# Kernel optimization log

Measured on AMD Instinct MI355X. Metric: run time of the kernel, lower is better.

Reference implementation:

```python
import jax, jax.numpy as jnp
import numpy as np

N = 256
D = 128
H = 512
EPS_NORM = 1e-12
EPS_COS = 1e-8


def _mlp2(x, w1, b1, w2, b2):
    return jax.nn.relu(x @ w1 + b1) @ w2 + b2


def _l2norm(x):
    n = jnp.sqrt(jnp.sum(x * x, axis=1, keepdims=True))
    return x / jnp.maximum(n, EPS_NORM)


def setup_inputs() -> dict:
    key = jax.random.key(0)
    ks = jax.random.split(key, 20)
    def w(k, shape, fan_in):
        return jax.random.normal(k, shape, dtype=jnp.float32) * (1.0 / np.sqrt(fan_in))
    inp = {
        "graph_1_node": jax.random.normal(ks[0], (N, D), dtype=jnp.float32),
        "graph_2_node": jax.random.normal(ks[1], (N, D), dtype=jnp.float32),
        # Node_embedding: D -> 512 -> D
        "ne_w1": w(ks[2], (D, H), D), "ne_b1": jnp.zeros((H,), jnp.float32),
        "ne_w2": w(ks[3], (H, D), H), "ne_b2": jnp.zeros((D,), jnp.float32),
        # edge_embedding: 2D+2N -> 512 -> D
        "ee_w1": w(ks[4], (2 * D + 2 * N, H), 2 * D + 2 * N), "ee_b1": jnp.zeros((H,), jnp.float32),
        "ee_w2": w(ks[5], (H, D), H), "ee_b2": jnp.zeros((D,), jnp.float32),
        # propagation: 3D -> 512 -> D
        "pr_w1": w(ks[6], (3 * D, H), 3 * D), "pr_b1": jnp.zeros((H,), jnp.float32),
        "pr_w2": w(ks[7], (H, D), H), "pr_b2": jnp.zeros((D,), jnp.float32),
        # update: 3D -> D (single linear)
        "up_w": w(ks[8], (3 * D, D), 3 * D), "up_b": jnp.zeros((D,), jnp.float32),
        # aggregation: 2D -> 1 (single linear, softmax over nodes)
        "ag_w": w(ks[9], (2 * D, 1), 2 * D), "ag_b": jnp.zeros((1,), jnp.float32),
    }
    return inp


def _edge_embed(x, ee_w1, ee_b1, ee_w2, ee_b2):
    # create_edg: per (i,j) concat(x[i], onehot(i), x[j], onehot(j))
    fi = jnp.concatenate([x, jnp.eye(N, dtype=x.dtype)], axis=1)  # [N, D+N]
    ef = jnp.concatenate([
        jnp.broadcast_to(fi[:, None, :], (N, N, D + N)),
        jnp.broadcast_to(fi[None, :, :], (N, N, D + N)),
    ], axis=-1).reshape(N * N, 2 * (D + N))
    return _mlp2(ef, ee_w1, ee_b1, ee_w2, ee_b2).reshape(N, N, D)


def _propagate(x, E, pr_w1, pr_b1, pr_w2, pr_b2):
    # msg[m] = mean_n MLP(cat(x[m], x[n], E[m,n]))
    cat = jnp.concatenate([
        jnp.broadcast_to(x[:, None, :], (N, N, D)),
        jnp.broadcast_to(x[None, :, :], (N, N, D)),
        E,
    ], axis=-1).reshape(N * N, 3 * D)
    msg = _mlp2(cat, pr_w1, pr_b1, pr_w2, pr_b2).reshape(N, N, D)
    return jnp.mean(msg, axis=1)


def _interact(a, b):
    # matching[i] = mean_j b[j] * exp(a[i]*b[j]) / sum_j (a[i]*b[j])
    p = a[:, None, :] * b[None, :, :]                      # [N, N, D]
    w = jnp.exp(p) / jnp.sum(p, axis=1, keepdims=True)
    return jnp.mean(b[None, :, :] * w, axis=1)


def _aggregate(upd, ag_w, ag_b):
    feats = jnp.concatenate([upd, jnp.broadcast_to(jnp.mean(upd, axis=0, keepdims=True), upd.shape)], axis=1)
    s = jax.nn.softmax(feats @ ag_w + ag_b, axis=0)        # [N, 1]
    return jnp.sum(s * upd, axis=0, keepdims=True)          # [1, D]


def reference(graph_1_node, graph_2_node,
              ne_w1, ne_b1, ne_w2, ne_b2,
              ee_w1, ee_b1, ee_w2, ee_b2,
              pr_w1, pr_b1, pr_w2, pr_b2,
              up_w, up_b, ag_w, ag_b):
    emb1 = _mlp2(graph_1_node, ne_w1, ne_b1, ne_w2, ne_b2)
    emb2 = _mlp2(graph_2_node, ne_w1, ne_b1, ne_w2, ne_b2)

    E1 = _edge_embed(graph_1_node, ee_w1, ee_b1, ee_w2, ee_b2)
    E2 = _edge_embed(graph_2_node, ee_w1, ee_b1, ee_w2, ee_b2)

    intra1 = _propagate(graph_1_node, E1, pr_w1, pr_b1, pr_w2, pr_b2)
    intra2 = _propagate(graph_2_node, E2, pr_w1, pr_b1, pr_w2, pr_b2)

    cross1 = _interact(emb1, emb2)
    cross2 = _interact(emb2, emb1)

    upd1 = jnp.concatenate([_l2norm(emb1), _l2norm(intra1), _l2norm(cross1)], axis=1) @ up_w + up_b
    upd2 = jnp.concatenate([_l2norm(emb2), _l2norm(intra2), _l2norm(cross2)], axis=1) @ up_w + up_b

    r1 = _aggregate(upd1, ag_w, ag_b)  # [1, D]
    r2 = _aggregate(upd2, ag_w, ag_b)  # [1, D]

    num = jnp.sum(r1 * r2, axis=1)
    den = jnp.maximum(jnp.linalg.norm(r1, axis=1) * jnp.linalg.norm(r2, axis=1), EPS_COS)
    return (num / den + 1.0) / 2.0
```

## Files before the change

kernel.cpp:

```cpp
#include <hip/hip_runtime.h>
#include <math.h>

#define NN 256
#define DD 128
#define HH 512

#define WS_XW    0
#define WS_XEXT  524288
#define WS_EMB   524288
#define WS_INTRA 589824
#define WS_W4F   720896
#define WS_UPD   720896
#define WS_H1    1114112
#define WS_S     1376256
#define WS_WB5   1638400
#define WS_B4    1802240
#define WS_LGV   1804288

typedef __attribute__((ext_vector_type(8))) _Float16 half8;
typedef __attribute__((ext_vector_type(4))) _Float16 half4v;
typedef __attribute__((ext_vector_type(4))) float f32x4;

__device__ __forceinline__ void gload_lds16(const _Float16* g, _Float16* l) {
  __builtin_amdgcn_global_load_lds(
      (const __attribute__((address_space(1))) unsigned*)g,
      (__attribute__((address_space(3))) unsigned*)l, 16, 0, 0);
}

#define WAITV(N) asm volatile("s_waitcnt vmcnt(" #N ")" ::: "memory")
#define RBARRIER() do { __builtin_amdgcn_s_barrier(); \
                        asm volatile("" ::: "memory"); } while (0)

__global__ void prepk(const float* __restrict__ g1, const float* __restrict__ g2,
                      const float* __restrict__ eew1, const float* __restrict__ prw1,
                      const float* __restrict__ eeb1, const float* __restrict__ prb1,
                      const float* __restrict__ eeb2, const float* __restrict__ eew2,
                      const float* __restrict__ new1, const float* __restrict__ new2,
                      const float* __restrict__ prw2,
                      float* __restrict__ Xext, _Float16* __restrict__ W4f,
                      _Float16* __restrict__ Wb5, float* __restrict__ bias4)
{
  const int b = blockIdx.x, l = threadIdx.x;
  const int low = l & 15, q = l >> 4;
  if (b < 1536) {
    const int f = b;
    const int kcI = f >> 7, ntI = f & 127;
    const int n = ntI * 16 + low, slice = n >> 9, np = n & 511;
    const int kb = kcI * 32 + q * 8;
    half8 v;
    #pragma unroll
    for (int t = 0; t < 8; ++t) {
      const int k = kb + t;
      float val;
      if (slice == 0)      val = eew1[k * HH + np];
      else if (slice == 1) val = eew1[(384 + k) * HH + np];
      else if (slice == 2) val = (k < 128) ? prw1[k * HH + np] : 0.f;
      else                 val = (k < 128) ? prw1[(128 + k) * HH + np] : 0.f;
      v[t] = (_Float16)val;
    }
    *(half8*)&W4f[((size_t)f * 64 + l) * 8] = v;
  } else if (b < 2176) {
    const int idx = b - 1536;
    const int which = idx >> 7, f = idx & 127;
    const float* src; int ld, nt;
    switch (which) {
      case 0:  src = eew2;            ld = 128; nt = 8;  break;
      case 1:  src = prw1 + 256 * HH; ld = 512; nt = 32; break;
      case 2:  src = new1;            ld = 512; nt = 32; break;
      case 3:  src = new2;            ld = 128; nt = 8;  break;
      default: src = prw2;            ld = 128; nt = 8;  break;
    }
    _Float16* dst = Wb5 + (size_t)which * 65536;
    const int kcI = f / nt, ntI = f % nt;
    const int n = ntI * 16 + low;
    const int kb = kcI * 32 + q * 8;
    half8 v;
    #pragma unroll
    for (int t = 0; t < 8; ++t) v[t] = (_Float16)src[(kb + t) * ld + n];
    *(half8*)&dst[((size_t)f * 64 + l) * 8] = v;
  } else if (b < 2688) {
    const int m = b - 2176;
    const int g = m >> 8, i = m & 255;
    const float* src = (g ? g2 : g1) + i * DD;
    float* dst = Xext + (size_t)m * 384;
    #pragma unroll
    for (int c = l; c < 384; c += 64)
      dst[c] = (c < 128) ? src[c] : ((c - 128 == i) ? 1.f : 0.f);
  } else {
    const int n = (b - 2688) * 64 + l;
    float v = 0.f;
    if (n < 512) v = eeb1[n];
    else if (n >= 1024 && n < 1536) {
      const int h = n - 1024;
      float s = prb1[h];
      #pragma unroll 8
      for (int d = 0; d < 128; ++d) s = fmaf(eeb2[d], prw1[(256 + d) * HH + h], s);
      v = s;
    }
    bias4[n] = v;
  }
}

template<int FT, int MT>
__global__ __launch_bounds__(256, 2)
void gemm2(const float* B0, const float* B1, int ldb0, int ldb1,
           float sc0, float sc1,
           const _Float16* A0, const _Float16* A1, int nt0, int nt1,
           int kcn0, int kcn1, const float* bias0, const float* bias1,
           void* O0, void* O1, int ldo0, int ldo1,
           int half0, int half1, int relu0, int relu1, int ylim1)
{
  const int z = blockIdx.z;
  if (z == 1 && (int)blockIdx.y >= ylim1) return;
  const float* Bsrc = z ? B1 : B0;
  const _Float16* Af = z ? A1 : A0;
  const float* bias = z ? bias1 : bias0;
  void* Out = z ? O1 : O0;
  const int ldb = z ? ldb1 : ldb0, ntTot = z ? nt1 : nt0;
  const int kcN = z ? kcn1 : kcn0, ldo = z ? ldo1 : ldo0;
  const int ohalf = z ? half1 : half0, orelu = z ? relu1 : relu0;
  const float sc = z ? sc1 : sc0;

  const int tid = threadIdx.x;
  const int w = tid >> 6, l = tid & 63, low = l & 15, q = l >> 4;
  const int mb = blockIdx.x * (MT * 16);
  const int nb = (blockIdx.y * 4 + w) * (FT * 16);
  f32x4 acc[FT][MT];
  #pragma unroll
  for (int ft = 0; ft < FT; ++ft)
    #pragma unroll
    for (int et = 0; et < MT; ++et) acc[ft][et] = (f32x4){0.f, 0.f, 0.f, 0.f};

  for (int kc = 0; kc < kcN; ++kc) {
    const int k0 = kc * 32 + q * 8;
    half8 bfr[MT];
    #pragma unroll
    for (int et = 0; et < MT; ++et) {
      const float* p = Bsrc + (size_t)(mb + et * 16 + low) * ldb + k0;
      const float4 b0 = *(const float4*)p;
      const float4 b1 = *(const float4*)(p + 4);
      half8 v;
      v[0] = (_Float16)(b0.x * sc); v[1] = (_Float16)(b0.y * sc);
      v[2] = (_Float16)(b0.z * sc); v[3] = (_Float16)(b0.w * sc);
      v[4] = (_Float16)(b1.x * sc); v[5] = (_Float16)(b1.y * sc);
      v[6] = (_Float16)(b1.z * sc); v[7] = (_Float16)(b1.w * sc);
      bfr[et] = v;
    }
    #pragma unroll
    for (int ft = 0; ft < FT; ++ft) {
      const int ng = (nb >> 4) + ft;
      const half8 af = *(const half8*)&Af[((size_t)(kc * ntTot + ng) * 64 + l) * 8];
      #pragma unroll
      for (int et = 0; et < MT; ++et)
        acc[ft][et] = __builtin_amdgcn_mfma_f32_16x16x32_f16(af, bfr[et], acc[ft][et], 0, 0, 0);
    }
  }
  #pragma unroll
  for (int ft = 0; ft < FT; ++ft) {
    const int n0 = nb + ft * 16 + q * 4;
    const float4 bs = *(const float4*)&bias[n0];
    #pragma unroll
    for (int et = 0; et < MT; ++et) {
      const int m = mb + et * 16 + low;
      float vx = acc[ft][et][0] + bs.x;
      float vy = acc[ft][et][1] + bs.y;
      float vz = acc[ft][et][2] + bs.z;
      float vw = acc[ft][et][3] + bs.w;
      if (orelu) {
        vx = fmaxf(vx, 0.f); vy = fmaxf(vy, 0.f);
        vz = fmaxf(vz, 0.f); vw = fmaxf(vw, 0.f);
      }
      if (ohalf) {
        half4v pk;
        pk[0] = (_Float16)vx; pk[1] = (_Float16)vy;
        pk[2] = (_Float16)vz; pk[3] = (_Float16)vw;
        *(half4v*)((_Float16*)Out + (size_t)m * ldo + n0) = pk;
      } else {
        *(float4*)((float*)Out + (size_t)m * ldo + n0) = make_float4(vx, vy, vz, vw);
      }
    }
  }
}

__global__ __launch_bounds__(512, 4)
void heavy_mfma(const _Float16* __restrict__ XW, const _Float16* __restrict__ W2fg,
                const _Float16* __restrict__ WEf, float* __restrict__ SG)
{
  __shared__ _Float16 Ut[128 * DD];
  __shared__ _Float16 Sb[3][4096];
  __shared__ _Float16 AeH[HH];
  __shared__ float PpL[HH];
  __shared__ float Sp[8][HH];
  const int g = blockIdx.z, i = blockIdx.x;
  const int tid = threadIdx.x;
  const _Float16* Xg = XW + (size_t)g * NN * 2048;
  const _Float16* rowI = Xg + (size_t)i * 2048;
  const int w = tid >> 6, l = tid & 63, low = l & 15, q = l >> 4;
  const int xsw = (low & 7) << 1;
  const half8 hz = (half8)((_Float16)0);

  AeH[tid] = rowI[tid];
  PpL[tid] = (float)rowI[1024 + tid];
  #pragma unroll
  for (int t = 0; t < 8; ++t) ((float*)Sp)[tid + t * 512] = 0.f;

  for (int h2 = 0; h2 < 2; ++h2) {
    const int jb = h2 * 128;
    const int j = jb + w * 16 + low;
    const int e = w * 16 + low;

    __syncthreads();
    gload_lds16(W2fg + (size_t)w * 512 + l * 8, &Sb[0][w * 512]);
    gload_lds16(W2fg + 4096 + (size_t)w * 512 + l * 8, &Sb[1][w * 512]);
    {
      half8 ce_cur = *(const half8*)&Xg[(size_t)j * 2048 + 512 + q * 8];
      f32x4 acc[8];
      #pragma unroll
      for (int ct = 0; ct < 8; ++ct) acc[ct] = (f32x4){0.f, 0.f, 0.f, 0.f};
      for (int kc = 0; kc < 16; ++kc) {
        half8 ce_nxt = hz;
        if (kc < 15)
          ce_nxt = *(const half8*)&Xg[(size_t)j * 2048 + 512 + (kc + 1) * 32 + q * 8];
        if (kc == 0)       WAITV(1);
        else if (kc == 15) WAITV(0);
        else               WAITV(2);
        RBARRIER();
        if (kc < 14)
          gload_lds16(W2fg + (size_t)(kc + 2) * 4096 + w * 512 + l * 8,
                      &Sb[(kc + 2) % 3][w * 512]);
        const half8 a = *(const half8*)&AeH[kc * 32 + q * 8];
        const half8 bfr = __builtin_elementwise_max(a + ce_cur, hz);
        const _Float16* sb = &Sb[kc % 3][0];
        __builtin_amdgcn_s_setprio(1);
        #pragma unroll
        for (int ct = 0; ct < 8; ++ct) {
          const half8 wf = *(const half8*)&sb[ct * 512 + l * 8];
          acc[ct] = __builtin_amdgcn_mfma_f32_16x16x32_f16(wf, bfr, acc[ct], 0, 0, 0);
        }
        __builtin_amdgcn_s_setprio(0);
        ce_cur = ce_nxt;
      }
      #pragma unroll
      for (int ct = 0; ct < 8; ++ct) {
        const int cb2 = ct * 4 + q;
        half4v pk;
        pk[0] = (_Float16)acc[ct][0]; pk[1] = (_Float16)acc[ct][1];
        pk[2] = (_Float16)acc[ct][2]; pk[3] = (_Float16)acc[ct][3];
        *(half4v*)&Ut[e * DD + ((cb2 ^ xsw) << 2)] = pk;
      }
    }

    __syncthreads();
    gload_lds16(WEf + (size_t)((w >> 1) * 32 + 0 + (w & 1)) * 512 + l * 8,
                &Sb[0][w * 512]);
    gload_lds16(WEf + (size_t)((w >> 1) * 32 + 2 + (w & 1)) * 512 + l * 8,
                &Sb[1][w * 512]);
    {
      half8 bfr2[4];
      #pragma unroll
      for (int kc2 = 0; kc2 < 4; ++kc2) {
        const int cb0 = kc2 * 8 + q * 2;
        bfr2[kc2] = *(const half8*)&Ut[e * DD + ((cb0 ^ xsw) << 2)];
      }
      const half4v onesv = {(_Float16)1.f, (_Float16)1.f, (_Float16)1.f, (_Float16)1.f};
      for (int cc = 0; cc < 16; ++cc) {
        if (cc == 15) WAITV(0);
        else          WAITV(1);
        RBARRIER();
        const _Float16* sb = &Sb[cc % 3][0];
        #pragma unroll
        for (int t = 0; t < 2; ++t) {
          const int hc = cc * 2 + t;
          const int h0 = hc * 16;
          f32x4 acc2 = (f32x4){0.f, 0.f, 0.f, 0.f};
          __builtin_amdgcn_s_setprio(1);
          #pragma unroll
          for (int kc2 = 0; kc2 < 4; ++kc2) {
            const half8 af = *(const half8*)&sb[(kc2 * 2 + t) * 512 + l * 8];
            acc2 = __builtin_amdgcn_mfma_f32_16x16x32_f16(bfr2[kc2], af, acc2, 0, 0, 0);
          }
          __builtin_amdgcn_s_setprio(0);
          const float pp = PpL[h0 + low];
          half4v rv;
          #pragma unroll
          for (int r = 0; r < 4; ++r) {
            const int jr = jb + w * 16 + q * 4 + r;
            const float qv = (float)Xg[(size_t)jr * 2048 + 1536 + h0 + low];
            rv[r] = (_Float16)fmaxf(pp + qv + acc2[r], 0.f);
          }
          f32x4 red = __builtin_amdgcn_mfma_f32_16x16x16f16(
              rv, onesv, (f32x4){0.f, 0.f, 0.f, 0.f}, 0, 0, 0);
          if (low == 0) {
            float4* sp = (float4*)&Sp[w][h0 + q * 4];
            float4 v = *sp;
            v.x += red[0]; v.y += red[1]; v.z += red[2]; v.w += red[3];
            *sp = v;
          }
        }
        if (cc < 14)
          gload_lds16(WEf + (size_t)((w >> 1) * 32 + 2 * (cc + 2) + (w & 1)) * 512 + l * 8,
                      &Sb[(cc + 2) % 3][w * 512]);
      }
    }
  }
  __syncthreads();
  float s = 0.f;
  #pragma unroll
  for (int w2 = 0; w2 < 8; ++w2) s += Sp[w2][tid];
  SG[((size_t)g * NN + i) * HH + tid] = s;
}

__global__ void interupd(const float* __restrict__ embG, const float* __restrict__ intraG,
                         const float* __restrict__ upw, const float* __restrict__ upb,
                         const float* __restrict__ agw,
                         float* __restrict__ updG, float* __restrict__ lgv)
{
  const int i = blockIdx.x, dir = blockIdx.y;
  const int tid = threadIdx.x, d = tid & 127, jc = tid >> 7;
  __shared__ float pN[4][DD], pS[4][DD], pdot[4][DD];
  __shared__ float vsm[3 * DD];
  __shared__ float pw[2][4];
  __shared__ float pw2[2];
  const float* A = embG + dir * NN * DD;
  const float* Bp = embG + (1 - dir) * NN * DD;
  const float av = A[i * DD + d];
  {
    float accN = 0.f, accS = 0.f;
    #pragma unroll 4
    for (int j = jc * 64; j < jc * 64 + 64; ++j) {
      const float bv = Bp[j * DD + d];
      accN = fmaf(bv, __expf(av * bv), accN);
      accS += bv;
    }
    pN[jc][d] = accN; pS[jc][d] = accS;
  }
  __syncthreads();
  float cv = 0.f, iv = 0.f;
  if (jc == 0) {
    const float accN = pN[0][d] + pN[1][d] + pN[2][d] + pN[3][d];
    const float accS = pS[0][d] + pS[1][d] + pS[2][d] + pS[3][d];
    cv = accN / (256.f * av * accS);
    iv = intraG[dir * NN * DD + i * DD + d];
    float q0 = av * av, q1 = iv * iv, q2 = cv * cv;
    #pragma unroll
    for (int st = 1; st < 64; st <<= 1) {
      q0 += __shfl_xor(q0, st);
      q1 += __shfl_xor(q1, st);
      q2 += __shfl_xor(q2, st);
    }
    const int w = d >> 6;
    if ((d & 63) == 0) { pw[w][0] = q0; pw[w][1] = q1; pw[w][2] = q2; }
  }
  __syncthreads();
  if (jc == 0) {
    const float n0 = 1.f / fmaxf(sqrtf(pw[0][0] + pw[1][0]), 1e-12f);
    const float n1 = 1.f / fmaxf(sqrtf(pw[0][1] + pw[1][1]), 1e-12f);
    const float n2 = 1.f / fmaxf(sqrtf(pw[0][2] + pw[1][2]), 1e-12f);
    vsm[d] = av * n0; vsm[DD + d] = iv * n1; vsm[2 * DD + d] = cv * n2;
  }
  __syncthreads();
  {
    float pd = (jc == 0) ? upb[d] : 0.f;
    #pragma unroll 8
    for (int k = jc * 96; k < jc * 96 + 96; ++k)
      pd = fmaf(vsm[k], upw[k * DD + d], pd);
    pdot[jc][d] = pd;
  }
  __syncthreads();
  if (jc == 0) {
    const float acc = pdot[0][d] + pdot[1][d] + pdot[2][d] + pdot[3][d];
    updG[dir * NN * DD + i * DD + d] = acc;
    float lp = acc * agw[d];
    #pragma unroll
    for (int st = 1; st < 64; st <<= 1) lp += __shfl_xor(lp, st);
    if ((d & 63) == 0) pw2[d >> 6] = lp;
  }
  __syncthreads();
  if (tid == 0) lgv[dir * NN + i] = pw2[0] + pw2[1];
}

__global__ void aggfin(const float* __restrict__ updG, const float* __restrict__ lgv,
                       float* __restrict__ out)
{
  __shared__ float mp[2][4][DD];
  __shared__ float sg[2][NN];
  __shared__ float redd[1024];
  const int t = threadIdx.x;
  const int g = t >> 9, tl = t & 511, jc = tl >> 7, d = tl & 127;
  const float* U = updG + g * NN * DD;
  const float lg = (tl < NN) ? lgv[g * NN + tl] : -1e30f;
  redd[t] = lg;
  __syncthreads();
  for (int st = 256; st > 0; st >>= 1) {
    if (tl < st) redd[t] = fmaxf(redd[t], redd[t + st]);
    __syncthreads();
  }
  const float mx = redd[g << 9];
  __syncthreads();
  const float e = (tl < NN) ? __expf(lg - mx) : 0.f;
  redd[t] = e;
  __syncthreads();
  for (int st = 256; st > 0; st >>= 1) {
    if (tl < st) redd[t] += redd[t + st];
    __syncthreads();
  }
  if (tl < NN) sg[g][tl] = e / redd[g << 9];
  __syncthreads();
  {
    float rp = 0.f;
    #pragma unroll 4
    for (int jj = jc * 64; jj < jc * 64 + 64; ++jj)
      rp = fmaf(sg[g][jj], U[jj * DD + d], rp);
    mp[g][jc][d] = rp;
  }
  __syncthreads();
  if (t < DD) {
    const float r0 = mp[0][0][t] + mp[0][1][t] + mp[0][2][t] + mp[0][3][t];
    const float r1 = mp[1][0][t] + mp[1][1][t] + mp[1][2][t] + mp[1][3][t];
    redd[t] = r0 * r1; redd[128 + t] = r0 * r0; redd[256 + t] = r1 * r1;
  }
  __syncthreads();
  for (int st = 64; st > 0; st >>= 1) {
    if (t < st) redd[t] += redd[t + st];
    else if (t >= 128 && t < 128 + st) redd[t] += redd[t + st];
    else if (t >= 256 && t < 256 + st) redd[t] += redd[t + st];
    __syncthreads();
  }
  if (t == 0)
    out[0] = (redd[0] / fmaxf(sqrtf(redd[128]) * sqrtf(redd[256]), 1e-8f) + 1.f) * 0.5f;
}

extern "C" void kernel_launch(void* const* d_in, const int* in_sizes, int n_in,
                              void* d_out, int out_size, void* d_ws, size_t ws_size,
                              hipStream_t stream)
{
  (void)in_sizes; (void)n_in; (void)out_size; (void)ws_size;
  const float* g1   = (const float*)d_in[0];
  const float* g2   = (const float*)d_in[1];
  const float* new1 = (const float*)d_in[2];
  const float* neb1 = (const float*)d_in[3];
  const float* new2 = (const float*)d_in[4];
  const float* neb2 = (const float*)d_in[5];
  const float* eew1 = (const float*)d_in[6];
  const float* eeb1 = (const float*)d_in[7];
  const float* eew2 = (const float*)d_in[8];
  const float* eeb2 = (const float*)d_in[9];
  const float* prw1 = (const float*)d_in[10];
  const float* prb1 = (const float*)d_in[11];
  const float* prw2 = (const float*)d_in[12];
  const float* prb2 = (const float*)d_in[13];
  const float* upw  = (const float*)d_in[14];
  const float* upb  = (const float*)d_in[15];
  const float* agw  = (const float*)d_in[16];
  const float* agb  = (const float*)d_in[17];
  (void)agb;
  float* W = (float*)d_ws;
  float* out = (float*)d_out;

  _Float16* XW16 = (_Float16*)(W + WS_XW);
  float* Xext    = W + WS_XEXT;
  float* emb     = W + WS_EMB;
  float* intra   = W + WS_INTRA;
  _Float16* W4f  = (_Float16*)(W + WS_W4F);
  float* updv    = W + WS_UPD;
  float* H1      = W + WS_H1;
  float* Sv      = W + WS_S;
  _Float16* Wb5  = (_Float16*)(W + WS_WB5);
  float* bias4   = W + WS_B4;
  float* lgv     = W + WS_LGV;
  _Float16* W2f  = Wb5;
  _Float16* WEf  = Wb5 + 65536;
  _Float16* W1nf = Wb5 + 2 * 65536;
  _Float16* W2nf = Wb5 + 3 * 65536;
  _Float16* PW2f = Wb5 + 4 * 65536;

  prepk<<<2720, 64, 0, stream>>>(g1, g2, eew1, prw1, eeb1, prb1, eeb2,
                                 eew2, new1, new2, prw2,
                                 Xext, W4f, Wb5, bias4);
  gemm2<2, 2><<<dim3(16, 16, 2), 256, 0, stream>>>(
      Xext, Xext, 384, 384, 1.f, 1.f,
      W4f, W1nf, 128, 32, 12, 4, bias4, neb1,
      (void*)XW16, (void*)H1, 2048, 512, 1, 0, 0, 1, 4);
  heavy_mfma<<<dim3(NN, 1, 2), 512, 0, stream>>>(XW16, W2f, WEf, Sv);
  gemm2<2, 1><<<dim3(32, 1, 2), 256, 0, stream>>>(
      H1, Sv, 512, 512, 1.f, 1.f / 256.f,
      W2nf, PW2f, 8, 8, 16, 16, neb2, prb2,
      (void*)emb, (void*)intra, 128, 128, 0, 0, 0, 0, 1);
  interupd<<<dim3(NN, 2), 512, 0, stream>>>(emb, intra, upw, upb, agw, updv, lgv);
  aggfin<<<1, 1024, 0, stream>>>(updv, lgv, out);
}
```

Baseline: 114.1 us.

## Process all 256 j-rows per pass so each LDS weight tile feeds two MFMAs

```diff
diff --git a/kernel.cpp b/kernel.cpp
--- a/kernel.cpp
+++ b/kernel.cpp
@@ -182,11 +182,11 @@
   }
 }
 
-__global__ __launch_bounds__(512, 4)
+__global__ __launch_bounds__(512, 2)
 void heavy_mfma(const _Float16* __restrict__ XW, const _Float16* __restrict__ W2fg,
                 const _Float16* __restrict__ WEf, float* __restrict__ SG)
 {
-  __shared__ _Float16 Ut[128 * DD];
+  __shared__ _Float16 Ut[NN * DD];
   __shared__ _Float16 Sb[3][4096];
   __shared__ _Float16 AeH[HH];
   __shared__ float PpL[HH];
@@ -198,108 +198,123 @@
   const int w = tid >> 6, l = tid & 63, low = l & 15, q = l >> 4;
   const int xsw = (low & 7) << 1;
   const half8 hz = (half8)((_Float16)0);
+  const int jA = w * 32 + low;
+  const int jB = w * 32 + 16 + low;
 
   AeH[tid] = rowI[tid];
   PpL[tid] = (float)rowI[1024 + tid];
   #pragma unroll
   for (int t = 0; t < 8; ++t) ((float*)Sp)[tid + t * 512] = 0.f;
-
-  for (int h2 = 0; h2 < 2; ++h2) {
-    const int jb = h2 * 128;
-    const int j = jb + w * 16 + low;
-    const int e = w * 16 + low;
-
-    __syncthreads();
-    gload_lds16(W2fg + (size_t)w * 512 + l * 8, &Sb[0][w * 512]);
-    gload_lds16(W2fg + 4096 + (size_t)w * 512 + l * 8, &Sb[1][w * 512]);
-    {
-      half8 ce_cur = *(const half8*)&Xg[(size_t)j * 2048 + 512 + q * 8];
-      f32x4 acc[8];
+  __syncthreads();
+  gload_lds16(W2fg + (size_t)w * 512 + l * 8, &Sb[0][w * 512]);
+  gload_lds16(W2fg + 4096 + (size_t)w * 512 + l * 8, &Sb[1][w * 512]);
+
+  {
+    half8 ceA = *(const half8*)&Xg[(size_t)jA * 2048 + 512 + q * 8];
+    half8 ceB = *(const half8*)&Xg[(size_t)jB * 2048 + 512 + q * 8];
+    f32x4 acc[8][2];
+    #pragma unroll
+    for (int ct = 0; ct < 8; ++ct) {
+      acc[ct][0] = (f32x4){0.f, 0.f, 0.f, 0.f};
+      acc[ct][1] = (f32x4){0.f, 0.f, 0.f, 0.f};
+    }
+    for (int kc = 0; kc < 16; ++kc) {
+      half8 ceA_n = hz, ceB_n = hz;
+      if (kc < 15) {
+        ceA_n = *(const half8*)&Xg[(size_t)jA * 2048 + 512 + (kc + 1) * 32 + q * 8];
+        ceB_n = *(const half8*)&Xg[(size_t)jB * 2048 + 512 + (kc + 1) * 32 + q * 8];
+      }
+      if (kc == 15) WAITV(0);
+      else          WAITV(3);
+      RBARRIER();
+      if (kc < 14)
+        gload_lds16(W2fg + (size_t)(kc + 2) * 4096 + w * 512 + l * 8,
+                    &Sb[(kc + 2) % 3][w * 512]);
+      const half8 a = *(const half8*)&AeH[kc * 32 + q * 8];
+      const half8 bfrA = __builtin_elementwise_max(a + ceA, hz);
+      const half8 bfrB = __builtin_elementwise_max(a + ceB, hz);
+      const _Float16* sb = &Sb[kc % 3][0];
+      __builtin_amdgcn_s_setprio(1);
       #pragma unroll
-      for (int ct = 0; ct < 8; ++ct) acc[ct] = (f32x4){0.f, 0.f, 0.f, 0.f};
-      for (int kc = 0; kc < 16; ++kc) {
-        half8 ce_nxt = hz;
-        if (kc < 15)
-          ce_nxt = *(const half8*)&Xg[(size_t)j * 2048 + 512 + (kc + 1) * 32 + q * 8];
-        if (kc == 0)       WAITV(1);
-        else if (kc == 15) WAITV(0);
-        else               WAITV(2);
-        RBARRIER();
-        if (kc < 14)
-          gload_lds16(W2fg + (size_t)(kc + 2) * 4096 + w * 512 + l * 8,
-                      &Sb[(kc + 2) % 3][w * 512]);
-        const half8 a = *(const half8*)&AeH[kc * 32 + q * 8];
-        const half8 bfr = __builtin_elementwise_max(a + ce_cur, hz);
-        const _Float16* sb = &Sb[kc % 3][0];
+      for (int ct = 0; ct < 8; ++ct) {
+        const half8 wf = *(const half8*)&sb[ct * 512 + l * 8];
+        acc[ct][0] = __builtin_amdgcn_mfma_f32_16x16x32_f16(wf, bfrA, acc[ct][0], 0, 0, 0);
+        acc[ct][1] = __builtin_amdgcn_mfma_f32_16x16x32_f16(wf, bfrB, acc[ct][1], 0, 0, 0);
+      }
+      __builtin_amdgcn_s_setprio(0);
+      ceA = ceA_n; ceB = ceB_n;
+    }
+    #pragma unroll
+    for (int ct = 0; ct < 8; ++ct) {
+      const int cb2 = ct * 4 + q;
+      #pragma unroll
+      for (int et = 0; et < 2; ++et) {
+        const int e = w * 32 + et * 16 + low;
+        half4v pk;
+        pk[0] = (_Float16)acc[ct][et][0]; pk[1] = (_Float16)acc[ct][et][1];
+        pk[2] = (_Float16)acc[ct][et][2]; pk[3] = (_Float16)acc[ct][et][3];
+        *(half4v*)&Ut[e * DD + ((cb2 ^ xsw) << 2)] = pk;
+      }
+    }
+  }
+
+  __syncthreads();
+  gload_lds16(WEf + (size_t)((w >> 1) * 32 + 0 + (w & 1)) * 512 + l * 8,
+              &Sb[0][w * 512]);
+  gload_lds16(WEf + (size_t)((w >> 1) * 32 + 2 + (w & 1)) * 512 + l * 8,
+              &Sb[1][w * 512]);
+  {
+    half8 bfr2[4][2];
+    #pragma unroll
+    for (int kc2 = 0; kc2 < 4; ++kc2) {
+      const int cb0 = kc2 * 8 + q * 2;
+      bfr2[kc2][0] = *(const half8*)&Ut[(w * 32 + low) * DD + ((cb0 ^ xsw) << 2)];
+      bfr2[kc2][1] = *(const half8*)&Ut[(w * 32 + 16 + low) * DD + ((cb0 ^ xsw) << 2)];
+    }
+    const half4v onesv = {(_Float16)1.f, (_Float16)1.f, (_Float16)1.f, (_Float16)1.f};
+    for (int cc = 0; cc < 16; ++cc) {
+      if (cc == 15) WAITV(0);
+      else          WAITV(1);
+      RBARRIER();
+      if (cc < 14)
+        gload_lds16(WEf + (size_t)((w >> 1) * 32 + 2 * (cc + 2) + (w & 1)) * 512 + l * 8,
+                    &Sb[(cc + 2) % 3][w * 512]);
+      const _Float16* sb = &Sb[cc % 3][0];
+      #pragma unroll
+      for (int t = 0; t < 2; ++t) {
+        const int hc = cc * 2 + t;
+        const int h0 = hc * 16;
+        f32x4 acc2[2];
+        acc2[0] = (f32x4){0.f, 0.f, 0.f, 0.f};
+        acc2[1] = (f32x4){0.f, 0.f, 0.f, 0.f};
         __builtin_amdgcn_s_setprio(1);
         #pragma unroll
-        for (int ct = 0; ct < 8; ++ct) {
-          const half8 wf = *(const half8*)&sb[ct * 512 + l * 8];
-          acc[ct] = __builtin_amdgcn_mfma_f32_16x16x32_f16(wf, bfr, acc[ct], 0, 0, 0);
+        for (int kc2 = 0; kc2 < 4; ++kc2) {
+          const half8 af = *(const half8*)&sb[(kc2 * 2 + t) * 512 + l * 8];
+          acc2[0] = __builtin_amdgcn_mfma_f32_16x16x32_f16(bfr2[kc2][0], af, acc2[0], 0, 0, 0);
+          acc2[1] = __builtin_amdgcn_mfma_f32_16x16x32_f16(bfr2[kc2][1], af, acc2[1], 0, 0, 0);
         }
         __builtin_amdgcn_s_setprio(0);
-        ce_cur = ce_nxt;
-      }
-      #pragma unroll
-      for (int ct = 0; ct < 8; ++ct) {
-        const int cb2 = ct * 4 + q;
-        half4v pk;
-        pk[0] = (_Float16)acc[ct][0]; pk[1] = (_Float16)acc[ct][1];
-        pk[2] = (_Float16)acc[ct][2]; pk[3] = (_Float16)acc[ct][3];
-        *(half4v*)&Ut[e * DD + ((cb2 ^ xsw) << 2)] = pk;
-      }
-    }
-
-    __syncthreads();
-    gload_lds16(WEf + (size_t)((w >> 1) * 32 + 0 + (w & 1)) * 512 + l * 8,
-                &Sb[0][w * 512]);
-    gload_lds16(WEf + (size_t)((w >> 1) * 32 + 2 + (w & 1)) * 512 + l * 8,
-                &Sb[1][w * 512]);
-    {
-      half8 bfr2[4];
-      #pragma unroll
-      for (int kc2 = 0; kc2 < 4; ++kc2) {
-        const int cb0 = kc2 * 8 + q * 2;
-        bfr2[kc2] = *(const half8*)&Ut[e * DD + ((cb0 ^ xsw) << 2)];
-      }
-      const half4v onesv = {(_Float16)1.f, (_Float16)1.f, (_Float16)1.f, (_Float16)1.f};
-      for (int cc = 0; cc < 16; ++cc) {
-        if (cc == 15) WAITV(0);
-        else          WAITV(1);
-        RBARRIER();
-        const _Float16* sb = &Sb[cc % 3][0];
+        const float pp = PpL[h0 + low];
+        half4v rv0, rv1;
         #pragma unroll
-        for (int t = 0; t < 2; ++t) {
-          const int hc = cc * 2 + t;
-          const int h0 = hc * 16;
-          f32x4 acc2 = (f32x4){0.f, 0.f, 0.f, 0.f};
-          __builtin_amdgcn_s_setprio(1);
-          #pragma unroll
-          for (int kc2 = 0; kc2 < 4; ++kc2) {
-            const half8 af = *(const half8*)&sb[(kc2 * 2 + t) * 512 + l * 8];
-            acc2 = __builtin_amdgcn_mfma_f32_16x16x32_f16(bfr2[kc2], af, acc2, 0, 0, 0);
-          }
-          __builtin_amdgcn_s_setprio(0);
-          const float pp = PpL[h0 + low];
-          half4v rv;
-          #pragma unroll
-          for (int r = 0; r < 4; ++r) {
-            const int jr = jb + w * 16 + q * 4 + r;
-            const float qv = (float)Xg[(size_t)jr * 2048 + 1536 + h0 + low];
-            rv[r] = (_Float16)fmaxf(pp + qv + acc2[r], 0.f);
-          }
-          f32x4 red = __builtin_amdgcn_mfma_f32_16x16x16f16(
-              rv, onesv, (f32x4){0.f, 0.f, 0.f, 0.f}, 0, 0, 0);
-          if (low == 0) {
-            float4* sp = (float4*)&Sp[w][h0 + q * 4];
-            float4 v = *sp;
-            v.x += red[0]; v.y += red[1]; v.z += red[2]; v.w += red[3];
-            *sp = v;
-          }
+        for (int r = 0; r < 4; ++r) {
+          const int jr0 = w * 32 + q * 4 + r;
+          const int jr1 = w * 32 + 16 + q * 4 + r;
+          const float qv0 = (float)Xg[(size_t)jr0 * 2048 + 1536 + h0 + low];
+          const float qv1 = (float)Xg[(size_t)jr1 * 2048 + 1536 + h0 + low];
+          rv0[r] = (_Float16)fmaxf(pp + qv0 + acc2[0][r], 0.f);
+          rv1[r] = (_Float16)fmaxf(pp + qv1 + acc2[1][r], 0.f);
         }
-        if (cc < 14)
-          gload_lds16(WEf + (size_t)((w >> 1) * 32 + 2 * (cc + 2) + (w & 1)) * 512 + l * 8,
-                      &Sb[(cc + 2) % 3][w * 512]);
+        f32x4 red = __builtin_amdgcn_mfma_f32_16x16x16f16(
+            rv0, onesv, (f32x4){0.f, 0.f, 0.f, 0.f}, 0, 0, 0);
+        red = __builtin_amdgcn_mfma_f32_16x16x16f16(rv1, onesv, red, 0, 0, 0);
+        if (low == 0) {
+          float4* sp = (float4*)&Sp[w][h0 + q * 4];
+          float4 v = *sp;
+          v.x += red[0]; v.y += red[1]; v.z += red[2]; v.w += red[3];
+          *sp = v;
+        }
       }
     }
   }
```

After: 126.7 us. 1.11x slower.
